# Performance work log

Hardware: AMD Instinct MI355X
Metric: run time of the kernel (lower is better)

Reference implementation:

```python
import jax, jax.numpy as jnp
import numpy as np

N_HEADS = 16
HEAD_DIM = 64
D_MODEL = N_HEADS * HEAD_DIM
MASK_NUM = -2.0**32 + 1.0
LN_EPS = 1e-8


def setup_inputs() -> dict:
    key = jax.random.key(0)
    ks = jax.random.split(key, 6)
    B, S = 2, 2048
    queries = jax.random.normal(ks[0], (B, S, D_MODEL), dtype=jnp.float32)
    keys = jax.random.normal(ks[1], (B, S, D_MODEL), dtype=jnp.float32)
    values = jax.random.normal(ks[2], (B, S, D_MODEL), dtype=jnp.float32)
    lim = np.sqrt(6.0 / (D_MODEL + D_MODEL)).astype(np.float32)  # glorot_uniform
    Wq = jax.random.uniform(ks[3], (D_MODEL, D_MODEL), jnp.float32, -lim, lim)
    Wk = jax.random.uniform(ks[4], (D_MODEL, D_MODEL), jnp.float32, -lim, lim)
    Wv = jax.random.uniform(ks[5], (D_MODEL, D_MODEL), jnp.float32, -lim, lim)
    gamma = jnp.ones((D_MODEL,), jnp.float32)
    beta = jnp.zeros((D_MODEL,), jnp.float32)
    return {"queries": queries, "keys": keys, "values": values,
            "Wq": Wq, "Wk": Wk, "Wv": Wv, "gamma": gamma, "beta": beta}


def _split_heads(x):
    # [B, S, H*dh] -> tf.split(axis=2)+concat(axis=0) order: [H*B, S, dh]
    B, S, _ = x.shape
    return x.reshape(B, S, N_HEADS, HEAD_DIM).transpose(2, 0, 1, 3).reshape(N_HEADS * B, S, HEAD_DIM)


def _merge_heads(x, B):
    # [H*B, S, dh] -> [B, S, H*dh]
    S = x.shape[1]
    return x.reshape(N_HEADS, B, S, HEAD_DIM).transpose(1, 2, 0, 3).reshape(B, S, D_MODEL)


def reference(queries, keys, values, Wq, Wk, Wv, gamma, beta):
    B = queries.shape[0]
    q = _split_heads(queries @ Wq)   # [HB, Sq, dh]
    k = _split_heads(keys @ Wk)      # [HB, Sk, dh]
    v = _split_heads(values @ Wv)    # [HB, Sk, dh]

    scores = jnp.einsum('bqd,bkd->bqk', q, k) / jnp.float32(np.sqrt(HEAD_DIM))
    # key padding mask: positions whose projected key is all-zero
    kmask = jnp.sign(jnp.sum(jnp.abs(k), axis=-1))  # [HB, Sk]
    scores = jnp.where(kmask[:, None, :] == 0, jnp.float32(MASK_NUM), scores)
    attn = jax.nn.softmax(scores, axis=-1)
    # query mask: zero out rows whose projected query is all-zero
    qmask = jnp.sign(jnp.sum(jnp.abs(q), axis=-1))  # [HB, Sq]
    attn = attn * qmask[:, :, None]
    att_out = jnp.einsum('bqk,bkd->bqd', attn, v)   # [HB, Sq, dh]
    att_out = _merge_heads(att_out, B)               # [B, Sq, D]

    x = att_out + queries
    mean = jnp.mean(x, axis=-1, keepdims=True)
    var = jnp.mean((x - mean) ** 2, axis=-1, keepdims=True)
    norm = (x - mean) / jnp.sqrt(var + LN_EPS)
    return gamma * norm + beta
```

## Files before the change

### kernel.cpp

```cpp
#include <hip/hip_runtime.h>

#define DM   1024
#define SEQ  2048
#define NH   16
#define HD   64
#define ROWS 4096

typedef unsigned short u16;
typedef unsigned int   u32;
typedef __attribute__((ext_vector_type(8))) __bf16 bf16x8;
typedef __attribute__((ext_vector_type(4))) float  f32x4;
typedef __attribute__((ext_vector_type(16))) float f32x16;

__device__ __forceinline__ u16 f2bf(float f) {
  u32 u = __builtin_bit_cast(u32, f);
  u += 0x7fffu + ((u >> 16) & 1u);
  return (u16)(u >> 16);
}

__device__ __forceinline__ void async16(const void* g, void* lds) {
  __builtin_amdgcn_global_load_lds((const __attribute__((address_space(1))) u32*)g,
                                   (__attribute__((address_space(3))) u32*)lds, 16, 0, 0);
}


__global__ __launch_bounds__(256) void k_cvt_act(const float* __restrict__ q,
                                                 const float* __restrict__ k,
                                                 const float* __restrict__ v,
                                                 u16* __restrict__ dst) {
  const float* src = blockIdx.z == 0 ? q : (blockIdx.z == 1 ? k : v);
  u16* d = dst + (size_t)blockIdx.z * ((size_t)ROWS * DM);
  size_t i = ((size_t)blockIdx.x * 256 + threadIdx.x) * 8;
  float4 a = *(const float4*)(src + i);
  float4 b = *(const float4*)(src + i + 4);
  u32 w0 = (u32)f2bf(a.x) | ((u32)f2bf(a.y) << 16);
  u32 w1 = (u32)f2bf(a.z) | ((u32)f2bf(a.w) << 16);
  u32 w2 = (u32)f2bf(b.x) | ((u32)f2bf(b.y) << 16);
  u32 w3 = (u32)f2bf(b.z) | ((u32)f2bf(b.w) << 16);
  uint4 o4; o4.x = w0; o4.y = w1; o4.z = w2; o4.w = w3;
  *(uint4*)(d + i) = o4;
}

__global__ __launch_bounds__(256) void k_cvt_wt(const float* __restrict__ Wq,
                                                const float* __restrict__ Wk,
                                                const float* __restrict__ Wv,
                                                u16* __restrict__ wt) {
  __shared__ float t[32][33];
  const float* W = blockIdx.z == 0 ? Wq : (blockIdx.z == 1 ? Wk : Wv);
  u16* D = wt + (size_t)blockIdx.z * (DM * DM);
  int bx = blockIdx.x * 32, by = blockIdx.y * 32;
  int x = threadIdx.x, y = threadIdx.y;
  for (int i = 0; i < 32; i += 8) t[y + i][x] = W[(size_t)(by + y + i) * DM + bx + x];
  __syncthreads();
  for (int i = 0; i < 32; i += 8) D[(size_t)(bx + y + i) * DM + by + x] = f2bf(t[x][y + i]);
}


__global__ __launch_bounds__(256) void k_gemm(const u16* __restrict__ Abase,
                                              const u16* __restrict__ Btbase,
                                              u16* __restrict__ Cbase) {
  __shared__ u16 As[128 * 32];
  __shared__ u16 Bs[128 * 32];
  const int z = blockIdx.z;
  const u16* A  = Abase  + (size_t)z * ((size_t)ROWS * DM);
  const u16* Bt = Btbase + (size_t)z * (DM * DM);
  u16* C        = Cbase  + (size_t)z * ((size_t)ROWS * DM);
  const float sc = (z == 0) ? 0.18033688011112043f : 1.0f;
  int tid = threadIdx.x, w = tid >> 6, l = tid & 63;
  int fr = l & 15, fq = l >> 4;
  int bid = blockIdx.y * 8 + blockIdx.x;
  int nb  = (bid & 7) * 32 + (bid >> 3);
  int m0 = (nb >> 3) * 128, n0 = (nb & 7) * 128;
  int wr = (w >> 1) * 64, wc = (w & 1) * 64;
  f32x4 acc[4][4];
  for (int i = 0; i < 4; ++i) for (int j = 0; j < 4; ++j) acc[i][j] = (f32x4){0.f, 0.f, 0.f, 0.f};

  for (int k0 = 0; k0 < DM; k0 += 32) {
    __syncthreads();
    for (int c = 0; c < 2; ++c) {
      int loff = (c * 4 + w) * 1024;
      int eoff = (loff >> 1) + l * 8;
      int row = eoff >> 5;
      int blk = (eoff & 31) >> 3;
      int gblk = blk ^ ((row >> 1) & 3);
      async16(A  + (size_t)(m0 + row) * DM + k0 + (gblk << 3), (char*)As + loff);
      async16(Bt + (size_t)(n0 + row) * DM + k0 + (gblk << 3), (char*)Bs + loff);
    }
    __syncthreads();
    bf16x8 af[4], bf[4];
    for (int i = 0; i < 4; ++i) {
      int row = wr + i * 16 + fr;
      af[i] = *(const bf16x8*)(As + row * 32 + ((fq ^ ((row >> 1) & 3)) << 3));
    }
    for (int j = 0; j < 4; ++j) {
      int row = wc + j * 16 + fr;
      bf[j] = *(const bf16x8*)(Bs + row * 32 + ((fq ^ ((row >> 1) & 3)) << 3));
    }
    for (int i = 0; i < 4; ++i)
      for (int j = 0; j < 4; ++j)
        acc[i][j] = __builtin_amdgcn_mfma_f32_16x16x32_bf16(af[i], bf[j], acc[i][j], 0, 0, 0);
  }
  for (int i = 0; i < 4; ++i)
    for (int j = 0; j < 4; ++j)
      for (int jj = 0; jj < 4; ++jj) {
        int row = m0 + wr + i * 16 + fq * 4 + jj;
        int col = n0 + wc + j * 16 + fr;
        C[(size_t)row * DM + col] = f2bf(acc[i][j][jj] * sc);
      }
}


__global__ __launch_bounds__(256) void k_vt(const u16* __restrict__ vproj,
                                            u16* __restrict__ vt) {
  __shared__ u16 t[64][64];
  int y = blockIdx.y;
  int h = y >> 1, b = y & 1;
  int s0 = blockIdx.x * 64;
  int tid = threadIdx.x;
  for (int c = 0; c < 2; ++c) {
    int rr = c * 32 + (tid >> 3);
    int blk = tid & 7;
    uint4 vv = *(const uint4*)(vproj + (size_t)(b * SEQ + s0 + rr) * DM + h * 64 + blk * 8);
    *(uint4*)(&t[rr][((blk ^ (rr & 7)) * 8)]) = vv;
  }
  __syncthreads();
  for (int c = 0; c < 2; ++c) {
    int d = c * 32 + (tid >> 3);
    int p = tid & 7;
    int B = p ^ (d & 7);
    int g = B >> 1, half = B & 1;
    u16 tmp[8];
    for (int j = 0; j < 8; ++j) {
      int kj = (j < 4) ? (4 * half + j) : (8 + 4 * half + (j - 4));
      int ss = 16 * g + kj;
      tmp[j] = t[ss][((d >> 3) ^ (ss & 7)) * 8 + (d & 7)];
    }
    *(uint4*)(vt + (size_t)(y * 64 + d) * SEQ + s0 + p * 8) = *(uint4*)tmp;
  }
}


__global__ __launch_bounds__(256, 4) void k_attn(const u16* __restrict__ Qp,
                                                 const u16* __restrict__ Kp,
                                                 const u16* __restrict__ Vt,
                                                 float* __restrict__ att) {
  __shared__ u16 lds[20480];
  const int tid = threadIdx.x, w = tid >> 6, l = tid & 63;
  const int lrow = l & 31, h = l >> 5;
  const int qh = w & 1, kh = w >> 1;
  const int g = blockIdx.x;
  const int vy = (g & 7) * 4 + ((g >> 3) & 3);
  const int vx = g >> 5;
  const int head = vy >> 1, b = vy & 1;
  const int hcol = head * 64;
  const int q0w = vx * 64 + qh * 32;

  const u16* qrow = Qp + (size_t)(b * SEQ + q0w + lrow) * DM + hcol + h * 8;
  bf16x8 qb0 = *(const bf16x8*)(qrow);
  bf16x8 qb1 = *(const bf16x8*)(qrow + 16);
  bf16x8 qb2 = *(const bf16x8*)(qrow + 32);
  bf16x8 qb3 = *(const bf16x8*)(qrow + 48);

  const int sw = lrow & 7;
  const int kbase = kh * 4096 + lrow * 128;
  const int B0 = kbase + (((0 + h) ^ sw) << 4);
  const int B1 = kbase + (((2 + h) ^ sw) << 4);
  const int B2 = kbase + (((4 + h) ^ sw) << 4);
  const int B3 = kbase + (((6 + h) ^ sw) << 4);

  const int vfb = lrow * 128;
  const int V0 = vfb + (((4 * kh + 0 + h) ^ sw) << 4);
  const int V1 = vfb + (((4 * kh + 2 + h) ^ sw) << 4);

  const int ldo0 = w * 1024, ldo1 = (4 + w) * 1024;
  const int e0 = (ldo0 >> 1) + l * 8, e1 = (ldo1 >> 1) + l * 8;
  const int r0 = e0 >> 6, r1 = e1 >> 6;
  const int kb0 = ((e0 & 63) >> 3) ^ (r0 & 7), kb1 = ((e1 & 63) >> 3) ^ (r1 & 7);
  const u32 koff0 = (u32)((b * SEQ + r0) * DM + hcol + kb0 * 8);
  const u32 koff1 = (u32)((b * SEQ + r1) * DM + hcol + kb1 * 8);
  const u32 voff0 = (u32)((vy * 64 + r0) * SEQ + (e0 & 63));
  const u32 voff1 = (u32)((vy * 64 + r1) * SEQ + (e1 & 63));

  const f32x16 kzero = {};
  f32x16 ot0 = {}, ot1 = {};
  float lacc = 0.f;
  bf16x8 pbP0 = {}, pbP1 = {};

  char* base = (char*)lds;
  async16(Kp + koff0, base + ldo0);
  async16(Kp + koff1, base + ldo1);
  async16(Vt + voff0, base + 16384 + ldo0);
  async16(Vt + voff1, base + 16384 + ldo1);

  int vwr = 1, vcr = 0, vrd = 2;
  for (int t = 0; t < SEQ / 64; ++t) {
    {
      u32 u = (t + 1 < SEQ / 64) ? (u32)(t + 1) : (u32)(SEQ / 64 - 1);
      u32 kadv = u * (64 * DM);
      u32 vadv = u * 64;
      char* kd = base + ((t + 1) & 1) * 8192;
      char* vd = base + 16384 + vwr * 8192;
      async16(Kp + kadv + koff0, kd + ldo0);
      async16(Kp + kadv + koff1, kd + ldo1);
      async16(Vt + vadv + voff0, vd + ldo0);
      async16(Vt + vadv + voff1, vd + ldo1);
    }
    asm volatile("s_waitcnt vmcnt(6)" ::: "memory");
    __builtin_amdgcn_s_barrier();
    asm volatile("" ::: "memory");

    const char* Kb = base + (t & 1) * 8192;
    bf16x8 a0 = *(const bf16x8*)(Kb + B0);
    bf16x8 a1 = *(const bf16x8*)(Kb + B1);
    bf16x8 a2 = *(const bf16x8*)(Kb + B2);
    bf16x8 a3 = *(const bf16x8*)(Kb + B3);
    __builtin_amdgcn_s_setprio(1);
    f32x16 st = __builtin_amdgcn_mfma_f32_32x32x16_bf16(a0, qb0, kzero, 0, 0, 0);
    st = __builtin_amdgcn_mfma_f32_32x32x16_bf16(a1, qb1, st, 0, 0, 0);
    st = __builtin_amdgcn_mfma_f32_32x32x16_bf16(a2, qb2, st, 0, 0, 0);
    st = __builtin_amdgcn_mfma_f32_32x32x16_bf16(a3, qb3, st, 0, 0, 0);
    __builtin_amdgcn_s_setprio(0);

    if (t) {
      const char* Vb = base + 16384 + vrd * 8192;
      bf16x8 vf0 = *(const bf16x8*)(Vb + V0);
      bf16x8 vf1 = *(const bf16x8*)(Vb + V1);
      bf16x8 vf2 = *(const bf16x8*)(Vb + 4096 + V0);
      bf16x8 vf3 = *(const bf16x8*)(Vb + 4096 + V1);
      __builtin_amdgcn_s_setprio(1);
      ot0 = __builtin_amdgcn_mfma_f32_32x32x16_bf16(vf0, pbP0, ot0, 0, 0, 0);
      ot0 = __builtin_amdgcn_mfma_f32_32x32x16_bf16(vf1, pbP1, ot0, 0, 0, 0);
      ot1 = __builtin_amdgcn_mfma_f32_32x32x16_bf16(vf2, pbP0, ot1, 0, 0, 0);
      ot1 = __builtin_amdgcn_mfma_f32_32x32x16_bf16(vf3, pbP1, ot1, 0, 0, 0);
      __builtin_amdgcn_s_setprio(0);
    }

    f32x16 p;
#pragma unroll
    for (int i = 0; i < 16; ++i) p[i] = __builtin_amdgcn_exp2f(st[i]);
    float s0 = (p[0] + p[1]) + (p[2] + p[3]);
    float s1 = (p[4] + p[5]) + (p[6] + p[7]);
    float s2 = (p[8] + p[9]) + (p[10] + p[11]);
    float s3 = (p[12] + p[13]) + (p[14] + p[15]);
    lacc += (s0 + s1) + (s2 + s3);
#pragma unroll
    for (int j = 0; j < 8; ++j) {
      pbP0[j] = (__bf16)p[j];
      pbP1[j] = (__bf16)p[8 + j];
    }

    asm volatile("" ::: "memory");
    __builtin_amdgcn_s_barrier();
    asm volatile("" ::: "memory");

    int tmp = vrd; vrd = vcr; vcr = vwr; vwr = tmp;
  }

  asm volatile("s_waitcnt vmcnt(0)" ::: "memory");
  __builtin_amdgcn_s_barrier();
  asm volatile("" ::: "memory");
  {
    const char* Vb = base + 16384 + vrd * 8192;
    bf16x8 vf0 = *(const bf16x8*)(Vb + V0);
    bf16x8 vf1 = *(const bf16x8*)(Vb + V1);
    bf16x8 vf2 = *(const bf16x8*)(Vb + 4096 + V0);
    bf16x8 vf3 = *(const bf16x8*)(Vb + 4096 + V1);
    ot0 = __builtin_amdgcn_mfma_f32_32x32x16_bf16(vf0, pbP0, ot0, 0, 0, 0);
    ot0 = __builtin_amdgcn_mfma_f32_32x32x16_bf16(vf1, pbP1, ot0, 0, 0, 0);
    ot1 = __builtin_amdgcn_mfma_f32_32x32x16_bf16(vf2, pbP0, ot1, 0, 0, 0);
    ot1 = __builtin_amdgcn_mfma_f32_32x32x16_bf16(vf3, pbP1, ot1, 0, 0, 0);
  }
  lacc += __shfl_xor(lacc, 32);

  __syncthreads();
  float* mrg = (float*)lds;
  const int slot = qh * 2176;
  if (kh) {
#pragma unroll
    for (int r = 0; r < 16; ++r) {
      mrg[slot + r * 64 + l] = ot0[r];
      mrg[slot + (16 + r) * 64 + l] = ot1[r];
    }
    mrg[slot + 2048 + l] = lacc;
  }
  __syncthreads();
  if (!kh) {
    float inv = 1.f / (lacc + mrg[slot + 2048 + l]);
    float* orow = att + (size_t)(b * SEQ + q0w + lrow) * DM + hcol + 4 * h;
#pragma unroll
    for (int G = 0; G < 4; ++G) {
      float4 w0;
      w0.x = (ot0[4 * G + 0] + mrg[slot + (4 * G + 0) * 64 + l]) * inv;
      w0.y = (ot0[4 * G + 1] + mrg[slot + (4 * G + 1) * 64 + l]) * inv;
      w0.z = (ot0[4 * G + 2] + mrg[slot + (4 * G + 2) * 64 + l]) * inv;
      w0.w = (ot0[4 * G + 3] + mrg[slot + (4 * G + 3) * 64 + l]) * inv;
      *(float4*)(orow + 8 * G) = w0;
      float4 w1;
      w1.x = (ot1[4 * G + 0] + mrg[slot + (16 + 4 * G + 0) * 64 + l]) * inv;
      w1.y = (ot1[4 * G + 1] + mrg[slot + (16 + 4 * G + 1) * 64 + l]) * inv;
      w1.z = (ot1[4 * G + 2] + mrg[slot + (16 + 4 * G + 2) * 64 + l]) * inv;
      w1.w = (ot1[4 * G + 3] + mrg[slot + (16 + 4 * G + 3) * 64 + l]) * inv;
      *(float4*)(orow + 32 + 8 * G) = w1;
    }
  }
}


__global__ __launch_bounds__(256) void k_ln(const float* __restrict__ att,
                                            const float* __restrict__ qin,
                                            const float* __restrict__ gamma,
                                            const float* __restrict__ beta,
                                            float* __restrict__ out) {
  __shared__ float rsum[4], rsum2[4];
  int row = blockIdx.x, t = threadIdx.x;
  size_t off = (size_t)row * DM + t * 4;
  float4 a = *(const float4*)(att + off);
  float4 q = *(const float4*)(qin + off);
  float4 x; x.x = a.x + q.x; x.y = a.y + q.y; x.z = a.z + q.z; x.w = a.w + q.w;
  float s = x.x + x.y + x.z + x.w;
  float s2 = x.x * x.x + x.y * x.y + x.z * x.z + x.w * x.w;
  for (int o2 = 1; o2 < 64; o2 <<= 1) { s += __shfl_xor(s, o2); s2 += __shfl_xor(s2, o2); }
  int w = t >> 6, l = t & 63;
  if (l == 0) { rsum[w] = s; rsum2[w] = s2; }
  __syncthreads();
  s = rsum[0] + rsum[1] + rsum[2] + rsum[3];
  s2 = rsum2[0] + rsum2[1] + rsum2[2] + rsum2[3];
  float mean = s * (1.f / DM);
  float var = s2 * (1.f / DM) - mean * mean;
  float rstd = rsqrtf(var + 1e-8f);
  float4 g = *(const float4*)(gamma + t * 4);
  float4 be = *(const float4*)(beta + t * 4);
  float4 r;
  r.x = (x.x - mean) * rstd * g.x + be.x;
  r.y = (x.y - mean) * rstd * g.y + be.y;
  r.z = (x.z - mean) * rstd * g.z + be.z;
  r.w = (x.w - mean) * rstd * g.w + be.w;
  *(float4*)(out + off) = r;
}


extern "C" void kernel_launch(void* const* d_in, const int* in_sizes, int n_in,
                              void* d_out, int out_size, void* d_ws, size_t ws_size,
                              hipStream_t stream) {
  (void)in_sizes; (void)n_in; (void)out_size; (void)ws_size;
  const float* q     = (const float*)d_in[0];
  const float* k     = (const float*)d_in[1];
  const float* v     = (const float*)d_in[2];
  const float* Wq    = (const float*)d_in[3];
  const float* Wk    = (const float*)d_in[4];
  const float* Wv    = (const float*)d_in[5];
  const float* gamma = (const float*)d_in[6];
  const float* beta  = (const float*)d_in[7];
  float* out = (float*)d_out;
  char* ws = (char*)d_ws;

  const size_t ACT_B = 3ull * ROWS * DM * 2;
  const size_t WT_B  = 3ull * DM * DM * 2;

  u16* actb  = (u16*)ws;
  u16* wtb   = (u16*)(ws + ACT_B);
  u16* projb = (u16*)(ws + ACT_B + WT_B);
  u16* vt    = (u16*)ws;
  float* att = (float*)(ws + 8ull * 1024 * 1024);

  k_cvt_act<<<dim3(2048, 1, 3), 256, 0, stream>>>(q, k, v, actb);
  k_cvt_wt<<<dim3(32, 32, 3), dim3(32, 8), 0, stream>>>(Wq, Wk, Wv, wtb);
  k_gemm<<<dim3(8, 32, 3), 256, 0, stream>>>(actb, wtb, projb);
  k_vt<<<dim3(SEQ / 64, NH * 2), 256, 0, stream>>>(projb + 2ull * ROWS * DM, vt);
  k_attn<<<1024, 256, 0, stream>>>(projb, projb + (size_t)ROWS * DM, vt, att);
  k_ln<<<ROWS, 256, 0, stream>>>(att, q, gamma, beta, out);
}
```

Before: 114.7 us.

## Process 128-key tiles per iteration with doubled LDS buffers in attention

New measurement: 116.6 us. No clear change (+1.6%).

```diff
diff --git a/kernel.cpp b/kernel.cpp
--- a/kernel.cpp
+++ b/kernel.cpp
@@ -140,20 +140,20 @@
 }
 
 
-__global__ __launch_bounds__(256, 4) void k_attn(const u16* __restrict__ Qp,
+__global__ __launch_bounds__(256, 2) void k_attn(const u16* __restrict__ Qp,
                                                  const u16* __restrict__ Kp,
                                                  const u16* __restrict__ Vt,
                                                  float* __restrict__ att) {
-  __shared__ u16 lds[20480];
+  __shared__ u16 lds[40960];
   const int tid = threadIdx.x, w = tid >> 6, l = tid & 63;
   const int lrow = l & 31, h = l >> 5;
-  const int qh = w & 1, kh = w >> 1;
+  const int kh = w & 1, qg = w >> 1;
   const int g = blockIdx.x;
   const int vy = (g & 7) * 4 + ((g >> 3) & 3);
   const int vx = g >> 5;
   const int head = vy >> 1, b = vy & 1;
   const int hcol = head * 64;
-  const int q0w = vx * 64 + qh * 32;
+  const int q0w = vx * 64 + qg * 32;
 
   const u16* qrow = Qp + (size_t)(b * SEQ + q0w + lrow) * DM + hcol + h * 8;
   bf16x8 qb0 = *(const bf16x8*)(qrow);
@@ -162,119 +162,148 @@
   bf16x8 qb3 = *(const bf16x8*)(qrow + 48);
 
   const int sw = lrow & 7;
-  const int kbase = kh * 4096 + lrow * 128;
-  const int B0 = kbase + (((0 + h) ^ sw) << 4);
-  const int B1 = kbase + (((2 + h) ^ sw) << 4);
-  const int B2 = kbase + (((4 + h) ^ sw) << 4);
-  const int B3 = kbase + (((6 + h) ^ sw) << 4);
-
-  const int vfb = lrow * 128;
-  const int V0 = vfb + (((4 * kh + 0 + h) ^ sw) << 4);
-  const int V1 = vfb + (((4 * kh + 2 + h) ^ sw) << 4);
-
-  const int ldo0 = w * 1024, ldo1 = (4 + w) * 1024;
-  const int e0 = (ldo0 >> 1) + l * 8, e1 = (ldo1 >> 1) + l * 8;
-  const int r0 = e0 >> 6, r1 = e1 >> 6;
-  const int kb0 = ((e0 & 63) >> 3) ^ (r0 & 7), kb1 = ((e1 & 63) >> 3) ^ (r1 & 7);
-  const u32 koff0 = (u32)((b * SEQ + r0) * DM + hcol + kb0 * 8);
-  const u32 koff1 = (u32)((b * SEQ + r1) * DM + hcol + kb1 * 8);
-  const u32 voff0 = (u32)((vy * 64 + r0) * SEQ + (e0 & 63));
-  const u32 voff1 = (u32)((vy * 64 + r1) * SEQ + (e1 & 63));
+  const int fb = kh * 8192 + lrow * 128;
+  const int F0 = fb + (((0 + h) ^ sw) << 4);
+  const int F1 = fb + (((2 + h) ^ sw) << 4);
+  const int F2 = fb + (((4 + h) ^ sw) << 4);
+  const int F3 = fb + (((6 + h) ^ sw) << 4);
+
+  u32 koff[4], voff[4];
+#pragma unroll
+  for (int i = 0; i < 4; ++i) {
+    int loff = (w * 4 + i) * 1024;
+    int e = (loff >> 1) + l * 8;
+    int krow = e >> 6;
+    int gblk = ((e & 63) >> 3) ^ (krow & 7);
+    koff[i] = (u32)((b * SEQ + krow) * DM + hcol + gblk * 8);
+    int ch = e >> 12;
+    int d  = (e >> 6) & 63;
+    voff[i] = (u32)((vy * 64 + d) * SEQ + ch * 64 + (e & 63));
+  }
 
   const f32x16 kzero = {};
   f32x16 ot0 = {}, ot1 = {};
   float lacc = 0.f;
-  bf16x8 pbP0 = {}, pbP1 = {};
+  bf16x8 pb00 = {}, pb01 = {}, pb10 = {}, pb11 = {};
 
   char* base = (char*)lds;
-  async16(Kp + koff0, base + ldo0);
-  async16(Kp + koff1, base + ldo1);
-  async16(Vt + voff0, base + 16384 + ldo0);
-  async16(Vt + voff1, base + 16384 + ldo1);
+#pragma unroll
+  for (int i = 0; i < 4; ++i) {
+    async16(Kp + koff[i], base + (w * 4 + i) * 1024);
+    async16(Vt + voff[i], base + 32768 + (w * 4 + i) * 1024);
+  }
+  __syncthreads();
 
   int vwr = 1, vcr = 0, vrd = 2;
-  for (int t = 0; t < SEQ / 64; ++t) {
+  for (int t = 0; t < SEQ / 128; ++t) {
+    if (t + 1 < SEQ / 128) {
+      u32 kadv = (u32)(t + 1) * (u32)(128 * DM);
+      u32 vadv = (u32)(t + 1) * 128u;
+      char* kd = base + ((t + 1) & 1) * 16384;
+      char* vd = base + 32768 + vwr * 16384;
+#pragma unroll
+      for (int i = 0; i < 4; ++i) {
+        async16(Kp + kadv + koff[i], kd + (w * 4 + i) * 1024);
+        async16(Vt + vadv + voff[i], vd + (w * 4 + i) * 1024);
+      }
+    }
+
+    const char* Kb = base + (t & 1) * 16384;
+    bf16x8 a0 = *(const bf16x8*)(Kb + F0);
+    bf16x8 a1 = *(const bf16x8*)(Kb + F1);
+    bf16x8 a2 = *(const bf16x8*)(Kb + F2);
+    bf16x8 a3 = *(const bf16x8*)(Kb + F3);
+    bf16x8 a4 = *(const bf16x8*)(Kb + 4096 + F0);
+    bf16x8 a5 = *(const bf16x8*)(Kb + 4096 + F1);
+    bf16x8 a6 = *(const bf16x8*)(Kb + 4096 + F2);
+    bf16x8 a7 = *(const bf16x8*)(Kb + 4096 + F3);
+    __builtin_amdgcn_s_setprio(1);
+    f32x16 st0 = __builtin_amdgcn_mfma_f32_32x32x16_bf16(a0, qb0, kzero, 0, 0, 0);
+    f32x16 st1 = __builtin_amdgcn_mfma_f32_32x32x16_bf16(a4, qb0, kzero, 0, 0, 0);
+    st0 = __builtin_amdgcn_mfma_f32_32x32x16_bf16(a1, qb1, st0, 0, 0, 0);
+    st1 = __builtin_amdgcn_mfma_f32_32x32x16_bf16(a5, qb1, st1, 0, 0, 0);
+    st0 = __builtin_amdgcn_mfma_f32_32x32x16_bf16(a2, qb2, st0, 0, 0, 0);
+    st1 = __builtin_amdgcn_mfma_f32_32x32x16_bf16(a6, qb2, st1, 0, 0, 0);
+    st0 = __builtin_amdgcn_mfma_f32_32x32x16_bf16(a3, qb3, st0, 0, 0, 0);
+    st1 = __builtin_amdgcn_mfma_f32_32x32x16_bf16(a7, qb3, st1, 0, 0, 0);
+    __builtin_amdgcn_s_setprio(0);
+
+    if (t) {
+      const char* Vb = base + 32768 + vrd * 16384;
+      bf16x8 vf0 = *(const bf16x8*)(Vb + F0);
+      bf16x8 vf1 = *(const bf16x8*)(Vb + F1);
+      bf16x8 vf2 = *(const bf16x8*)(Vb + F2);
+      bf16x8 vf3 = *(const bf16x8*)(Vb + F3);
+      bf16x8 vf4 = *(const bf16x8*)(Vb + 4096 + F0);
+      bf16x8 vf5 = *(const bf16x8*)(Vb + 4096 + F1);
+      bf16x8 vf6 = *(const bf16x8*)(Vb + 4096 + F2);
+      bf16x8 vf7 = *(const bf16x8*)(Vb + 4096 + F3);
+      __builtin_amdgcn_s_setprio(1);
+      ot0 = __builtin_amdgcn_mfma_f32_32x32x16_bf16(vf0, pb00, ot0, 0, 0, 0);
+      ot1 = __builtin_amdgcn_mfma_f32_32x32x16_bf16(vf4, pb00, ot1, 0, 0, 0);
+      ot0 = __builtin_amdgcn_mfma_f32_32x32x16_bf16(vf1, pb01, ot0, 0, 0, 0);
+      ot1 = __builtin_amdgcn_mfma_f32_32x32x16_bf16(vf5, pb01, ot1, 0, 0, 0);
+      ot0 = __builtin_amdgcn_mfma_f32_32x32x16_bf16(vf2, pb10, ot0, 0, 0, 0);
+      ot1 = __builtin_amdgcn_mfma_f32_32x32x16_bf16(vf6, pb10, ot1, 0, 0, 0);
+      ot0 = __builtin_amdgcn_mfma_f32_32x32x16_bf16(vf3, pb11, ot0, 0, 0, 0);
+      ot1 = __builtin_amdgcn_mfma_f32_32x32x16_bf16(vf7, pb11, ot1, 0, 0, 0);
+      __builtin_amdgcn_s_setprio(0);
+    }
+
     {
-      u32 u = (t + 1 < SEQ / 64) ? (u32)(t + 1) : (u32)(SEQ / 64 - 1);
-      u32 kadv = u * (64 * DM);
-      u32 vadv = u * 64;
-      char* kd = base + ((t + 1) & 1) * 8192;
-      char* vd = base + 16384 + vwr * 8192;
-      async16(Kp + kadv + koff0, kd + ldo0);
-      async16(Kp + kadv + koff1, kd + ldo1);
-      async16(Vt + vadv + voff0, vd + ldo0);
-      async16(Vt + vadv + voff1, vd + ldo1);
-    }
-    asm volatile("s_waitcnt vmcnt(6)" ::: "memory");
-    __builtin_amdgcn_s_barrier();
-    asm volatile("" ::: "memory");
-
-    const char* Kb = base + (t & 1) * 8192;
-    bf16x8 a0 = *(const bf16x8*)(Kb + B0);
-    bf16x8 a1 = *(const bf16x8*)(Kb + B1);
-    bf16x8 a2 = *(const bf16x8*)(Kb + B2);
-    bf16x8 a3 = *(const bf16x8*)(Kb + B3);
-    __builtin_amdgcn_s_setprio(1);
-    f32x16 st = __builtin_amdgcn_mfma_f32_32x32x16_bf16(a0, qb0, kzero, 0, 0, 0);
-    st = __builtin_amdgcn_mfma_f32_32x32x16_bf16(a1, qb1, st, 0, 0, 0);
-    st = __builtin_amdgcn_mfma_f32_32x32x16_bf16(a2, qb2, st, 0, 0, 0);
-    st = __builtin_amdgcn_mfma_f32_32x32x16_bf16(a3, qb3, st, 0, 0, 0);
-    __builtin_amdgcn_s_setprio(0);
-
-    if (t) {
-      const char* Vb = base + 16384 + vrd * 8192;
-      bf16x8 vf0 = *(const bf16x8*)(Vb + V0);
-      bf16x8 vf1 = *(const bf16x8*)(Vb + V1);
-      bf16x8 vf2 = *(const bf16x8*)(Vb + 4096 + V0);
-      bf16x8 vf3 = *(const bf16x8*)(Vb + 4096 + V1);
-      __builtin_amdgcn_s_setprio(1);
-      ot0 = __builtin_amdgcn_mfma_f32_32x32x16_bf16(vf0, pbP0, ot0, 0, 0, 0);
-      ot0 = __builtin_amdgcn_mfma_f32_32x32x16_bf16(vf1, pbP1, ot0, 0, 0, 0);
-      ot1 = __builtin_amdgcn_mfma_f32_32x32x16_bf16(vf2, pbP0, ot1, 0, 0, 0);
-      ot1 = __builtin_amdgcn_mfma_f32_32x32x16_bf16(vf3, pbP1, ot1, 0, 0, 0);
-      __builtin_amdgcn_s_setprio(0);
-    }
-
-    f32x16 p;
-#pragma unroll
-    for (int i = 0; i < 16; ++i) p[i] = __builtin_amdgcn_exp2f(st[i]);
-    float s0 = (p[0] + p[1]) + (p[2] + p[3]);
-    float s1 = (p[4] + p[5]) + (p[6] + p[7]);
-    float s2 = (p[8] + p[9]) + (p[10] + p[11]);
-    float s3 = (p[12] + p[13]) + (p[14] + p[15]);
-    lacc += (s0 + s1) + (s2 + s3);
-#pragma unroll
-    for (int j = 0; j < 8; ++j) {
-      pbP0[j] = (__bf16)p[j];
-      pbP1[j] = (__bf16)p[8 + j];
-    }
-
-    asm volatile("" ::: "memory");
-    __builtin_amdgcn_s_barrier();
-    asm volatile("" ::: "memory");
+      f32x16 p;
+#pragma unroll
+      for (int i = 0; i < 16; ++i) p[i] = __builtin_amdgcn_exp2f(st0[i]);
+      float s0 = (p[0] + p[1]) + (p[2] + p[3]);
+      float s1 = (p[4] + p[5]) + (p[6] + p[7]);
+      float s2 = (p[8] + p[9]) + (p[10] + p[11]);
+      float s3 = (p[12] + p[13]) + (p[14] + p[15]);
+      lacc += (s0 + s1) + (s2 + s3);
+#pragma unroll
+      for (int j = 0; j < 8; ++j) { pb00[j] = (__bf16)p[j]; pb01[j] = (__bf16)p[8 + j]; }
+    }
+    {
+      f32x16 p;
+#pragma unroll
+      for (int i = 0; i < 16; ++i) p[i] = __builtin_amdgcn_exp2f(st1[i]);
+      float s0 = (p[0] + p[1]) + (p[2] + p[3]);
+      float s1 = (p[4] + p[5]) + (p[6] + p[7]);
+      float s2 = (p[8] + p[9]) + (p[10] + p[11]);
+      float s3 = (p[12] + p[13]) + (p[14] + p[15]);
+      lacc += (s0 + s1) + (s2 + s3);
+#pragma unroll
+      for (int j = 0; j < 8; ++j) { pb10[j] = (__bf16)p[j]; pb11[j] = (__bf16)p[8 + j]; }
+    }
+
+    __syncthreads();
 
     int tmp = vrd; vrd = vcr; vcr = vwr; vwr = tmp;
   }
 
-  asm volatile("s_waitcnt vmcnt(0)" ::: "memory");
-  __builtin_amdgcn_s_barrier();
-  asm volatile("" ::: "memory");
   {
-    const char* Vb = base + 16384 + vrd * 8192;
-    bf16x8 vf0 = *(const bf16x8*)(Vb + V0);
-    bf16x8 vf1 = *(const bf16x8*)(Vb + V1);
-    bf16x8 vf2 = *(const bf16x8*)(Vb + 4096 + V0);
-    bf16x8 vf3 = *(const bf16x8*)(Vb + 4096 + V1);
-    ot0 = __builtin_amdgcn_mfma_f32_32x32x16_bf16(vf0, pbP0, ot0, 0, 0, 0);
-    ot0 = __builtin_amdgcn_mfma_f32_32x32x16_bf16(vf1, pbP1, ot0, 0, 0, 0);
-    ot1 = __builtin_amdgcn_mfma_f32_32x32x16_bf16(vf2, pbP0, ot1, 0, 0, 0);
-    ot1 = __builtin_amdgcn_mfma_f32_32x32x16_bf16(vf3, pbP1, ot1, 0, 0, 0);
+    const char* Vb = base + 32768 + vrd * 16384;
+    bf16x8 vf0 = *(const bf16x8*)(Vb + F0);
+    bf16x8 vf1 = *(const bf16x8*)(Vb + F1);
+    bf16x8 vf2 = *(const bf16x8*)(Vb + F2);
+    bf16x8 vf3 = *(const bf16x8*)(Vb + F3);
+    bf16x8 vf4 = *(const bf16x8*)(Vb + 4096 + F0);
+    bf16x8 vf5 = *(const bf16x8*)(Vb + 4096 + F1);
+    bf16x8 vf6 = *(const bf16x8*)(Vb + 4096 + F2);
+    bf16x8 vf7 = *(const bf16x8*)(Vb + 4096 + F3);
+    ot0 = __builtin_amdgcn_mfma_f32_32x32x16_bf16(vf0, pb00, ot0, 0, 0, 0);
+    ot1 = __builtin_amdgcn_mfma_f32_32x32x16_bf16(vf4, pb00, ot1, 0, 0, 0);
+    ot0 = __builtin_amdgcn_mfma_f32_32x32x16_bf16(vf1, pb01, ot0, 0, 0, 0);
+    ot1 = __builtin_amdgcn_mfma_f32_32x32x16_bf16(vf5, pb01, ot1, 0, 0, 0);
+    ot0 = __builtin_amdgcn_mfma_f32_32x32x16_bf16(vf2, pb10, ot0, 0, 0, 0);
+    ot1 = __builtin_amdgcn_mfma_f32_32x32x16_bf16(vf6, pb10, ot1, 0, 0, 0);
+    ot0 = __builtin_amdgcn_mfma_f32_32x32x16_bf16(vf3, pb11, ot0, 0, 0, 0);
+    ot1 = __builtin_amdgcn_mfma_f32_32x32x16_bf16(vf7, pb11, ot1, 0, 0, 0);
   }
   lacc += __shfl_xor(lacc, 32);
 
   __syncthreads();
   float* mrg = (float*)lds;
-  const int slot = qh * 2176;
+  const int slot = qg * 2176;
   if (kh) {
 #pragma unroll
     for (int r = 0; r < 16; ++r) {
```
